# Kernel optimization log

Measured on AMD Instinct MI355X. Metric: run time of the kernel, lower is better.

Reference implementation:

```python
import jax, jax.numpy as jnp
import numpy as np

VOCAB, EMBED, UNITS, BATCH, SEQ = 32000, 1024, 1024, 64, 128


def _lstm_layer(x, mask, Wx, Wh, b):
    """Keras-style LSTM (gate order i, f, g, o) with zero-masking semantics.
    x: [B, T, D], mask: [B, T] bool. Returns (seq [B,T,U], h [B,U], c [B,U])."""
    B, T, _ = x.shape
    U = Wh.shape[0]
    # Precompute input projection for all timesteps (big GEMM, compute-bound).
    xp = jnp.einsum('btd,dg->btg', x, Wx) + b            # [B, T, 4U]
    xp_t = jnp.transpose(xp, (1, 0, 2))                  # [T, B, 4U]
    mask_t = jnp.transpose(mask, (1, 0))                 # [T, B]

    def step(carry, inp):
        h, c = carry
        xt, mt = inp
        z = xt + h @ Wh                                  # [B, 4U]
        i = jax.nn.sigmoid(z[:, :U])
        f = jax.nn.sigmoid(z[:, U:2 * U])
        g = jnp.tanh(z[:, 2 * U:3 * U])
        o = jax.nn.sigmoid(z[:, 3 * U:])
        c_new = f * c + i * g
        h_new = o * jnp.tanh(c_new)
        m = mt[:, None]
        h2 = jnp.where(m, h_new, h)   # masked steps carry state/output through
        c2 = jnp.where(m, c_new, c)
        return (h2, c2), h2

    h0 = jnp.zeros((B, U), x.dtype)
    c0 = jnp.zeros((B, U), x.dtype)
    (h, c), seq_t = jax.lax.scan(step, (h0, c0), (xp_t, mask_t))
    return jnp.transpose(seq_t, (1, 0, 2)), h, c


def setup_inputs() -> dict:
    key = jax.random.key(0)
    ks = jax.random.split(key, 8)
    inputs = jax.random.randint(ks[0], (BATCH, SEQ), 0, VOCAB, dtype=jnp.int32)
    emb = jax.random.uniform(ks[1], (VOCAB, EMBED), jnp.float32, -0.05, 0.05)
    s_in = 1.0 / np.sqrt(EMBED)
    s_u = 1.0 / np.sqrt(UNITS)
    Wx0 = jax.random.normal(ks[2], (EMBED, 4 * UNITS), jnp.float32) * s_in
    Wh0 = jax.random.normal(ks[3], (UNITS, 4 * UNITS), jnp.float32) * s_u
    b0 = jnp.zeros((4 * UNITS,), jnp.float32).at[UNITS:2 * UNITS].set(1.0)  # unit_forget_bias
    Wx1 = jax.random.normal(ks[4], (UNITS, 4 * UNITS), jnp.float32) * s_u
    Wh1 = jax.random.normal(ks[5], (UNITS, 4 * UNITS), jnp.float32) * s_u
    b1 = jnp.zeros((4 * UNITS,), jnp.float32).at[UNITS:2 * UNITS].set(1.0)
    return {"inputs": inputs, "emb": emb, "Wx0": Wx0, "Wh0": Wh0, "b0": b0,
            "Wx1": Wx1, "Wh1": Wh1, "b1": b1}


def reference(inputs, emb, Wx0, Wh0, b0, Wx1, Wh1, b1):
    mask = inputs != 0                              # mask_zero=True
    x = emb[inputs]                                 # [B, T, E]
    seq, h0_, c0_ = _lstm_layer(x, mask, Wx0, Wh0, b0)
    seq, h1_, c1_ = _lstm_layer(seq, mask, Wx1, Wh1, b1)
    return seq, h0_, c0_, h1_, c1_
```

## Files before the change

### kernel.cpp

```cpp
#include <hip/hip_runtime.h>
#include <hip/hip_bf16.h>
#include <cstdint>
#include <cstddef>

typedef __attribute__((ext_vector_type(8))) short bf16x8;
typedef __attribute__((ext_vector_type(4))) float f32x4;
typedef __attribute__((ext_vector_type(4))) unsigned int u32x4;

__device__ __forceinline__ unsigned short f2bf(float f) {
  unsigned u = __float_as_uint(f);
  return (unsigned short)((u + 0x7fffu + ((u >> 16) & 1u)) >> 16);
}

__global__ __launch_bounds__(256) void transpose_cast_k(const float* __restrict__ W,
                                                        unsigned short* __restrict__ WT) {
  __shared__ float tile[32][33];
  const int bn = blockIdx.x * 32, bk = blockIdx.y * 32;
  const int tx = threadIdx.x & 31, ty = threadIdx.x >> 5;
#pragma unroll
  for (int i = 0; i < 4; ++i) {
    const int k = ty + i * 8;
    tile[k][tx] = W[(size_t)(bk + k) * 4096 + bn + tx];
  }
  __syncthreads();
#pragma unroll
  for (int i = 0; i < 4; ++i) {
    const int n = ty + i * 8;
    WT[(size_t)(bn + n) * 1024 + bk + tx] = f2bf(tile[tx][n]);
  }
}

__global__ __launch_bounds__(256) void embed_gather_k(const int* __restrict__ ids,
                                                      const float* __restrict__ emb,
                                                      unsigned short* __restrict__ x) {
  const int bt = blockIdx.x;
  const int id = ids[bt];
  const float4 v = ((const float4*)(emb + (size_t)id * 1024))[threadIdx.x];
  union { unsigned short u[4]; unsigned long long ll; } o;
  o.u[0] = f2bf(v.x); o.u[1] = f2bf(v.y); o.u[2] = f2bf(v.z); o.u[3] = f2bf(v.w);
  *(unsigned long long*)(x + (size_t)bt * 1024 + threadIdx.x * 4) = o.ll;
}

__global__ __launch_bounds__(256) void gemm_bt_k(const unsigned short* __restrict__ A,
                                                 const unsigned short* __restrict__ BT,
                                                 const float* __restrict__ bias,
                                                 float* __restrict__ C) {
  __shared__ char sA[128 * 128];
  __shared__ char sB[128 * 128];
  const int bid = blockIdx.x;
  const int bm = (bid >> 5) * 128;
  const int bn = (bid & 31) * 128;
  const int tid = threadIdx.x, lane = tid & 63;
  const int wv = tid >> 6, wm = wv >> 1, wn = wv & 1;
  const int lrow = lane & 15, lk = (lane >> 4) * 16;
  f32x4 acc[4][4] = {};
  for (int kt = 0; kt < 16; ++kt) {
    const int k0 = kt * 64;
    bf16x8 av[4], bv[4];
#pragma unroll
    for (int i = 0; i < 4; ++i) {
      const int ch = i * 256 + tid;
      const int row = ch >> 3, c = ch & 7;
      av[i] = *(const bf16x8*)(A + (size_t)(bm + row) * 1024 + k0 + c * 8);
      bv[i] = *(const bf16x8*)(BT + (size_t)(bn + row) * 1024 + k0 + c * 8);
    }
    __syncthreads();
#pragma unroll
    for (int i = 0; i < 4; ++i) {
      const int ch = i * 256 + tid;
      const int row = ch >> 3, c = ch & 7;
      const int off = row * 128 + ((c * 16) ^ ((row & 7) << 4));
      *(bf16x8*)(sA + off) = av[i];
      *(bf16x8*)(sB + off) = bv[i];
    }
    __syncthreads();
#pragma unroll
    for (int kk = 0; kk < 2; ++kk) {
      bf16x8 af[4], bf_[4];
#pragma unroll
      for (int mi = 0; mi < 4; ++mi) {
        const int row = wm * 64 + mi * 16 + lrow;
        af[mi] = *(const bf16x8*)(sA + row * 128 + ((kk * 64 + lk) ^ ((row & 7) << 4)));
      }
#pragma unroll
      for (int ni = 0; ni < 4; ++ni) {
        const int row = wn * 64 + ni * 16 + lrow;
        bf_[ni] = *(const bf16x8*)(sB + row * 128 + ((kk * 64 + lk) ^ ((row & 7) << 4)));
      }
#pragma unroll
      for (int mi = 0; mi < 4; ++mi)
#pragma unroll
        for (int ni = 0; ni < 4; ++ni)
          acc[mi][ni] = __builtin_amdgcn_mfma_f32_16x16x32_bf16(af[mi], bf_[ni], acc[mi][ni], 0, 0, 0);
    }
  }
  const int cr0 = (lane >> 4) * 4;
#pragma unroll
  for (int mi = 0; mi < 4; ++mi)
#pragma unroll
    for (int ni = 0; ni < 4; ++ni) {
      const int col = bn + wn * 64 + ni * 16 + lrow;
      const float bb = bias[col];
#pragma unroll
      for (int r = 0; r < 4; ++r) {
        const int row = bm + wm * 64 + mi * 16 + cr0 + r;
        C[(size_t)row * 4096 + col] = acc[mi][ni][r] + bb;
      }
    }
}

template <int LAYER>
__global__ __launch_bounds__(256) void lstm_layer_k(
    const float* __restrict__ xp,
    const unsigned short* __restrict__ WhT,
    const int* __restrict__ ids,
    unsigned short* __restrict__ hbuf,
    unsigned short* __restrict__ seqbf,
    float* __restrict__ seqf,
    float* __restrict__ hfin, float* __restrict__ cfin,
    unsigned* __restrict__ flags_all) {
  extern __shared__ __align__(16) char dlds[];
  char* wlds = dlds;
  float* zp = (float*)(dlds + 131072);
  const int tid = threadIdx.x, lane = tid & 63, wave = tid >> 6;
  const int wg = blockIdx.x;
  const int g = wg & 3, w = wg >> 2;
  const int b0 = g * 16, u0 = w * 16;
  unsigned* flags = flags_all + g * 1024;

  for (int i = 0; i < 32; ++i) {
    const int ch = i * 256 + tid;
    const int n = ch >> 7, c = ch & 127;
    const int grow = (n >> 4) * 1024 + u0 + (n & 15);
    bf16x8 v = *(const bf16x8*)(WhT + (size_t)grow * 1024 + c * 8);
    *(bf16x8*)(wlds + n * 2048 + ((c * 16) ^ ((n & 7) << 4))) = v;
  }
  const int rrow = tid >> 4, du = tid & 15;
  const int brow = b0 + rrow, unit = u0 + du;
  {
    unsigned short* p = hbuf + (size_t)brow * 1024 + unit;
    unsigned zv = 0;
    asm volatile("global_store_short %0, %1, off sc0 sc1" :: "v"(p), "v"(zv) : "memory");
  }
  asm volatile("s_waitcnt vmcnt(0)" ::: "memory");
  __syncthreads();
  if (tid == 0)
    __hip_atomic_store(&flags[w * 16], 1u, __ATOMIC_RELAXED, __HIP_MEMORY_SCOPE_AGENT);

  float c_reg = 0.f, h_reg = 0.f;
  const int lr = lane & 15;
  const int lkb = (lane >> 4) * 16;
  const int wq = wave * 512;

  for (int t = 0; t < 128; ++t) {
    const float* xr = xp + ((size_t)brow * 128 + t) * 4096 + unit;
    const float x0 = xr[0], x1 = xr[1024], x2 = xr[2048], x3 = xr[3072];
    const int idv = ids[brow * 128 + t];
    {
      const unsigned* fp = flags + lane * 16;
      const unsigned target = (unsigned)(t + 1);
      for (;;) {
        unsigned v = __hip_atomic_load(fp, __ATOMIC_RELAXED, __HIP_MEMORY_SCOPE_AGENT);
        if (__all((int)(v >= target))) break;
        __builtin_amdgcn_s_sleep(1);
      }
    }
    const char* hb = (const char*)hbuf + (size_t)(t & 1) * 131072 +
                     (size_t)(b0 + lr) * 2048 + wq + lkb;
    u32x4 araw[8];
#pragma unroll
    for (int c = 0; c < 8; ++c)
      asm volatile("global_load_dwordx4 %0, %1, off sc0 sc1"
                   : "=&v"(araw[c]) : "v"(hb + c * 64) : "memory");
    asm volatile("s_waitcnt vmcnt(0)" ::: "memory");
    __builtin_amdgcn_sched_barrier(0);
    f32x4 acc[4] = {};
#pragma unroll
    for (int gg = 0; gg < 4; ++gg) {
      const int n = gg * 16 + lr;
      const char* bb = wlds + n * 2048;
      const int bx = (n & 7) << 4;
#pragma unroll
      for (int c = 0; c < 8; ++c) {
        bf16x8 bfv = *(const bf16x8*)(bb + ((wq + c * 64 + lkb) ^ bx));
        acc[gg] = __builtin_amdgcn_mfma_f32_16x16x32_bf16(
            __builtin_bit_cast(bf16x8, araw[c]), bfv, acc[gg], 0, 0, 0);
      }
    }
    const int zr0 = (lane >> 4) * 4;
#pragma unroll
    for (int gg = 0; gg < 4; ++gg)
#pragma unroll
      for (int r = 0; r < 4; ++r)
        zp[((wave * 4 + gg) * 16 + zr0 + r) * 20 + lr] = acc[gg][r];
    __syncthreads();
    float zg0 = x0, zg1 = x1, zg2 = x2, zg3 = x3;
#pragma unroll
    for (int ww = 0; ww < 4; ++ww) {
      zg0 += zp[((ww * 4 + 0) * 16 + rrow) * 20 + du];
      zg1 += zp[((ww * 4 + 1) * 16 + rrow) * 20 + du];
      zg2 += zp[((ww * 4 + 2) * 16 + rrow) * 20 + du];
      zg3 += zp[((ww * 4 + 3) * 16 + rrow) * 20 + du];
    }
    const float ig = 1.f / (1.f + __expf(-zg0));
    const float fg = 1.f / (1.f + __expf(-zg1));
    const float gt = 1.f - 2.f / (1.f + __expf(2.f * zg2));
    const float og = 1.f / (1.f + __expf(-zg3));
    const float cn = fg * c_reg + ig * gt;
    const float hn = og * (1.f - 2.f / (1.f + __expf(2.f * cn)));
    if (idv != 0) { c_reg = cn; h_reg = hn; }
    const unsigned short hb16 = f2bf(h_reg);
    {
      unsigned short* p = hbuf + (size_t)((t & 1) ^ 1) * 65536 + (size_t)brow * 1024 + unit;
      asm volatile("global_store_short %0, %1, off sc0 sc1"
                   :: "v"(p), "v"((unsigned)hb16) : "memory");
    }
    if (LAYER == 0)
      seqbf[((size_t)brow * 128 + t) * 1024 + unit] = hb16;
    else
      seqf[((size_t)brow * 128 + t) * 1024 + unit] = h_reg;
    asm volatile("s_waitcnt vmcnt(0)" ::: "memory");
    __syncthreads();
    if (tid == 0)
      __hip_atomic_store(&flags[w * 16], (unsigned)(t + 2), __ATOMIC_RELAXED,
                         __HIP_MEMORY_SCOPE_AGENT);
  }
  hfin[(size_t)brow * 1024 + unit] = h_reg;
  cfin[(size_t)brow * 1024 + unit] = c_reg;
}

extern "C" void kernel_launch(void* const* d_in, const int* in_sizes, int n_in,
                              void* d_out, int out_size, void* d_ws, size_t ws_size,
                              hipStream_t stream) {
  (void)in_sizes; (void)n_in; (void)out_size; (void)ws_size;
  const int* ids = (const int*)d_in[0];
  const float* emb = (const float*)d_in[1];
  const float* Wx0 = (const float*)d_in[2];
  const float* Wh0 = (const float*)d_in[3];
  const float* b0 = (const float*)d_in[4];
  const float* Wx1 = (const float*)d_in[5];
  const float* Wh1 = (const float*)d_in[6];
  const float* b1 = (const float*)d_in[7];
  float* out = (float*)d_out;

  char* ws = (char*)d_ws;
  const size_t SZ_WT = (size_t)4096 * 1024 * 2;
  unsigned short* WxT0 = (unsigned short*)(ws);
  unsigned short* WhT0 = (unsigned short*)(ws + SZ_WT);
  unsigned short* WxT1 = (unsigned short*)(ws + 2 * SZ_WT);
  unsigned short* WhT1 = (unsigned short*)(ws + 3 * SZ_WT);
  unsigned short* xbf = (unsigned short*)(ws + 4 * SZ_WT);
  unsigned short* seq0 = (unsigned short*)(ws + 4 * SZ_WT + 16777216);
  unsigned short* hbuf = (unsigned short*)(ws + 4 * SZ_WT + 2 * 16777216);
  unsigned* flags = (unsigned*)(ws + 4 * SZ_WT + 2 * 16777216 + 262144);
  float* xpb = (float*)(ws + 4 * SZ_WT + 2 * 16777216 + 262144 + 16384);

  float* h0f = out + 8388608;
  float* c0f = h0f + 65536;
  float* h1f = c0f + 65536;
  float* c1f = h1f + 65536;

  transpose_cast_k<<<dim3(128, 32), dim3(256), 0, stream>>>(Wx0, WxT0);
  transpose_cast_k<<<dim3(128, 32), dim3(256), 0, stream>>>(Wh0, WhT0);
  transpose_cast_k<<<dim3(128, 32), dim3(256), 0, stream>>>(Wx1, WxT1);
  transpose_cast_k<<<dim3(128, 32), dim3(256), 0, stream>>>(Wh1, WhT1);
  embed_gather_k<<<dim3(8192), dim3(256), 0, stream>>>(ids, emb, xbf);
  gemm_bt_k<<<dim3(2048), dim3(256), 0, stream>>>(xbf, WxT0, b0, xpb);

  hipFuncSetAttribute(reinterpret_cast<const void*>(&lstm_layer_k<0>),
                      hipFuncAttributeMaxDynamicSharedMemorySize, 151552);
  hipFuncSetAttribute(reinterpret_cast<const void*>(&lstm_layer_k<1>),
                      hipFuncAttributeMaxDynamicSharedMemorySize, 151552);

  hipMemsetAsync(flags, 0, 16384, stream);
  {
    const float* xp_p = xpb;
    const unsigned short* wht = WhT0;
    const int* ids_p = ids;
    unsigned short* hb_p = hbuf;
    unsigned short* sb_p = seq0;
    float* sf_p = nullptr;
    float* hf_p = h0f;
    float* cf_p = c0f;
    unsigned* fl_p = flags;
    void* ka[9] = {&xp_p, &wht, &ids_p, &hb_p, &sb_p, &sf_p, &hf_p, &cf_p, &fl_p};
    hipLaunchCooperativeKernel(reinterpret_cast<const void*>(&lstm_layer_k<0>),
                               dim3(256), dim3(256), ka, 151552u, stream);
  }
  gemm_bt_k<<<dim3(2048), dim3(256), 0, stream>>>(seq0, WxT1, b1, xpb);
  hipMemsetAsync(flags, 0, 16384, stream);
  {
    const float* xp_p = xpb;
    const unsigned short* wht = WhT1;
    const int* ids_p = ids;
    unsigned short* hb_p = hbuf;
    unsigned short* sb_p = nullptr;
    float* sf_p = out;
    float* hf_p = h1f;
    float* cf_p = c1f;
    unsigned* fl_p = flags;
    void* ka[9] = {&xp_p, &wht, &ids_p, &hb_p, &sb_p, &sf_p, &hf_p, &cf_p, &fl_p};
    hipLaunchCooperativeKernel(reinterpret_cast<const void*>(&lstm_layer_k<1>),
                               dim3(256), dim3(256), ka, 151552u, stream);
  }
}
```

Measured before the change: 1.388 ms.

## Replace flag-based step sync with self-validating h packets carrying step tags

The per-step cross-workgroup handshake moves off separate flag words. Each h value is now published as a 16-byte packet holding four bf16 hidden units plus a step tag. Consumers poll the packets directly and reload only those whose tag is stale, then stage the h tile through LDS for the MFMA. This drops the separate flag store/poll round trip, the vmcnt wait before each flag publish and the flag memsets. In exchange it doubles the size of the h exchange buffer, adds extra LDS staging and block barriers, and leaves the gate math on a single wave that handles four units per lane.

```diff
diff --git a/kernel.cpp b/kernel.cpp
--- a/kernel.cpp
+++ b/kernel.cpp
@@ -6,6 +6,7 @@
 typedef __attribute__((ext_vector_type(8))) short bf16x8;
 typedef __attribute__((ext_vector_type(4))) float f32x4;
 typedef __attribute__((ext_vector_type(4))) unsigned int u32x4;
+typedef __attribute__((ext_vector_type(2))) unsigned int u32x2;
 
 __device__ __forceinline__ unsigned short f2bf(float f) {
   unsigned u = __float_as_uint(f);
@@ -114,19 +115,19 @@
     const float* __restrict__ xp,
     const unsigned short* __restrict__ WhT,
     const int* __restrict__ ids,
-    unsigned short* __restrict__ hbuf,
+    u32x4* __restrict__ pktbuf,
     unsigned short* __restrict__ seqbf,
     float* __restrict__ seqf,
-    float* __restrict__ hfin, float* __restrict__ cfin,
-    unsigned* __restrict__ flags_all) {
+    float* __restrict__ hfin, float* __restrict__ cfin) {
   extern __shared__ __align__(16) char dlds[];
   char* wlds = dlds;
-  float* zp = (float*)(dlds + 131072);
+  char* htile = dlds + 131072;
+  float* zp = (float*)htile;
   const int tid = threadIdx.x, lane = tid & 63, wave = tid >> 6;
   const int wg = blockIdx.x;
   const int g = wg & 3, w = wg >> 2;
   const int b0 = g * 16, u0 = w * 16;
-  unsigned* flags = flags_all + g * 1024;
+  constexpr unsigned EB = LAYER * 512u;
 
   for (int i = 0; i < 32; ++i) {
     const int ch = i * 256 + tid;
@@ -135,45 +136,69 @@
     bf16x8 v = *(const bf16x8*)(WhT + (size_t)grow * 1024 + c * 8);
     *(bf16x8*)(wlds + n * 2048 + ((c * 16) ^ ((n & 7) << 4))) = v;
   }
-  const int rrow = tid >> 4, du = tid & 15;
-  const int brow = b0 + rrow, unit = u0 + du;
-  {
-    unsigned short* p = hbuf + (size_t)brow * 1024 + unit;
-    unsigned zv = 0;
-    asm volatile("global_store_short %0, %1, off sc0 sc1" :: "v"(p), "v"(zv) : "memory");
-  }
-  asm volatile("s_waitcnt vmcnt(0)" ::: "memory");
+
+  const int prow = lane >> 2, pk4 = lane & 3;
+  const int brow = b0 + prow;
+  const int myunit = u0 + pk4 * 4;
+  float cc[4] = {0.f, 0.f, 0.f, 0.f}, hh[4] = {0.f, 0.f, 0.f, 0.f};
+
+  if (wave == 0) {
+    u32x4 z; z[0] = 0u; z[1] = 0u; z[2] = EB + 1u; z[3] = 0u;
+    u32x4* p = pktbuf + (size_t)brow * 256 + (u0 >> 2) + pk4;
+    asm volatile("global_store_dwordx4 %0, %1, off sc0 sc1" :: "v"(p), "v"(z) : "memory");
+  }
   __syncthreads();
-  if (tid == 0)
-    __hip_atomic_store(&flags[w * 16], 1u, __ATOMIC_RELAXED, __HIP_MEMORY_SCOPE_AGENT);
-
-  float c_reg = 0.f, h_reg = 0.f;
-  const int lr = lane & 15;
-  const int lkb = (lane >> 4) * 16;
-  const int wq = wave * 512;
+
+  const int crow = tid >> 4;
+  const int cpk0 = tid & 15;
+  const int lr = lane & 15, lkb = (lane >> 4) * 16, wq = wave * 512;
+  const int asw = (lr & 7) << 4;
 
   for (int t = 0; t < 128; ++t) {
-    const float* xr = xp + ((size_t)brow * 128 + t) * 4096 + unit;
-    const float x0 = xr[0], x1 = xr[1024], x2 = xr[2048], x3 = xr[3072];
-    const int idv = ids[brow * 128 + t];
-    {
-      const unsigned* fp = flags + lane * 16;
-      const unsigned target = (unsigned)(t + 1);
-      for (;;) {
-        unsigned v = __hip_atomic_load(fp, __ATOMIC_RELAXED, __HIP_MEMORY_SCOPE_AGENT);
-        if (__all((int)(v >= target))) break;
-        __builtin_amdgcn_s_sleep(1);
-      }
-    }
-    const char* hb = (const char*)hbuf + (size_t)(t & 1) * 131072 +
-                     (size_t)(b0 + lr) * 2048 + wq + lkb;
-    u32x4 araw[8];
+    __syncthreads();
+    f32x4 xq0 = {}, xq1 = {}, xq2 = {}, xq3 = {};
+    int idv = 0;
+    if (wave == 0) {
+      const float* xr = xp + ((size_t)brow * 128 + t) * 4096 + myunit;
+      xq0 = *(const f32x4*)(xr);
+      xq1 = *(const f32x4*)(xr + 1024);
+      xq2 = *(const f32x4*)(xr + 2048);
+      xq3 = *(const f32x4*)(xr + 3072);
+      idv = ids[brow * 128 + t];
+    }
+    const unsigned target = EB + (unsigned)t + 1u;
+    const char* pb = (const char*)pktbuf + (size_t)(t & 1) * 262144 +
+                     ((size_t)(b0 + crow) * 256 + cpk0) * 16;
+    u32x4 pkt[16];
+#pragma unroll
+    for (int i = 0; i < 16; ++i)
+      asm volatile("global_load_dwordx4 %0, %1, off sc0 sc1"
+                   : "=&v"(pkt[i]) : "v"(pb + i * 256) : "memory");
+    asm volatile("s_waitcnt vmcnt(0)" ::: "memory");
+    for (;;) {
+      bool again = false;
+#pragma unroll
+      for (int i = 0; i < 16; ++i)
+        if (pkt[i][2] != target) {
+          asm volatile("global_load_dwordx4 %0, %1, off sc0 sc1"
+                       : "=&v"(pkt[i]) : "v"(pb + i * 256) : "memory");
+          again = true;
+        }
+      if (!again) break;
+      asm volatile("s_waitcnt vmcnt(0)" ::: "memory");
+    }
+    __builtin_amdgcn_sched_barrier(0);
+#pragma unroll
+    for (int i = 0; i < 16; ++i) {
+      const int pk = cpk0 + 16 * i;
+      u32x2 v; v[0] = pkt[i][0]; v[1] = pkt[i][1];
+      *(u32x2*)(htile + crow * 2048 + ((pk * 8) ^ ((crow & 7) << 4))) = v;
+    }
+    __syncthreads();
+    bf16x8 af[8];
 #pragma unroll
     for (int c = 0; c < 8; ++c)
-      asm volatile("global_load_dwordx4 %0, %1, off sc0 sc1"
-                   : "=&v"(araw[c]) : "v"(hb + c * 64) : "memory");
-    asm volatile("s_waitcnt vmcnt(0)" ::: "memory");
-    __builtin_amdgcn_sched_barrier(0);
+      af[c] = *(const bf16x8*)(htile + lr * 2048 + ((wq + c * 64 + lkb) ^ asw));
     f32x4 acc[4] = {};
 #pragma unroll
     for (int gg = 0; gg < 4; ++gg) {
@@ -183,10 +208,10 @@
 #pragma unroll
       for (int c = 0; c < 8; ++c) {
         bf16x8 bfv = *(const bf16x8*)(bb + ((wq + c * 64 + lkb) ^ bx));
-        acc[gg] = __builtin_amdgcn_mfma_f32_16x16x32_bf16(
-            __builtin_bit_cast(bf16x8, araw[c]), bfv, acc[gg], 0, 0, 0);
-      }
-    }
+        acc[gg] = __builtin_amdgcn_mfma_f32_16x16x32_bf16(af[c], bfv, acc[gg], 0, 0, 0);
+      }
+    }
+    __syncthreads();
     const int zr0 = (lane >> 4) * 4;
 #pragma unroll
     for (int gg = 0; gg < 4; ++gg)
@@ -194,39 +219,47 @@
       for (int r = 0; r < 4; ++r)
         zp[((wave * 4 + gg) * 16 + zr0 + r) * 20 + lr] = acc[gg][r];
     __syncthreads();
-    float zg0 = x0, zg1 = x1, zg2 = x2, zg3 = x3;
-#pragma unroll
-    for (int ww = 0; ww < 4; ++ww) {
-      zg0 += zp[((ww * 4 + 0) * 16 + rrow) * 20 + du];
-      zg1 += zp[((ww * 4 + 1) * 16 + rrow) * 20 + du];
-      zg2 += zp[((ww * 4 + 2) * 16 + rrow) * 20 + du];
-      zg3 += zp[((ww * 4 + 3) * 16 + rrow) * 20 + du];
-    }
-    const float ig = 1.f / (1.f + __expf(-zg0));
-    const float fg = 1.f / (1.f + __expf(-zg1));
-    const float gt = 1.f - 2.f / (1.f + __expf(2.f * zg2));
-    const float og = 1.f / (1.f + __expf(-zg3));
-    const float cn = fg * c_reg + ig * gt;
-    const float hn = og * (1.f - 2.f / (1.f + __expf(2.f * cn)));
-    if (idv != 0) { c_reg = cn; h_reg = hn; }
-    const unsigned short hb16 = f2bf(h_reg);
-    {
-      unsigned short* p = hbuf + (size_t)((t & 1) ^ 1) * 65536 + (size_t)brow * 1024 + unit;
-      asm volatile("global_store_short %0, %1, off sc0 sc1"
-                   :: "v"(p), "v"((unsigned)hb16) : "memory");
-    }
-    if (LAYER == 0)
-      seqbf[((size_t)brow * 128 + t) * 1024 + unit] = hb16;
-    else
-      seqf[((size_t)brow * 128 + t) * 1024 + unit] = h_reg;
-    asm volatile("s_waitcnt vmcnt(0)" ::: "memory");
-    __syncthreads();
-    if (tid == 0)
-      __hip_atomic_store(&flags[w * 16], (unsigned)(t + 2), __ATOMIC_RELAXED,
-                         __HIP_MEMORY_SCOPE_AGENT);
-  }
-  hfin[(size_t)brow * 1024 + unit] = h_reg;
-  cfin[(size_t)brow * 1024 + unit] = c_reg;
+    if (wave == 0) {
+      f32x4 zs0 = xq0, zs1 = xq1, zs2 = xq2, zs3 = xq3;
+#pragma unroll
+      for (int ww = 0; ww < 4; ++ww) {
+        zs0 += *(const f32x4*)(zp + ((ww * 4 + 0) * 16 + prow) * 20 + pk4 * 4);
+        zs1 += *(const f32x4*)(zp + ((ww * 4 + 1) * 16 + prow) * 20 + pk4 * 4);
+        zs2 += *(const f32x4*)(zp + ((ww * 4 + 2) * 16 + prow) * 20 + pk4 * 4);
+        zs3 += *(const f32x4*)(zp + ((ww * 4 + 3) * 16 + prow) * 20 + pk4 * 4);
+      }
+#pragma unroll
+      for (int u = 0; u < 4; ++u) {
+        const float ig = 1.f / (1.f + __expf(-zs0[u]));
+        const float fg = 1.f / (1.f + __expf(-zs1[u]));
+        const float gt = 1.f - 2.f / (1.f + __expf(2.f * zs2[u]));
+        const float og = 1.f / (1.f + __expf(-zs3[u]));
+        const float cn = fg * cc[u] + ig * gt;
+        const float hn = og * (1.f - 2.f / (1.f + __expf(2.f * cn)));
+        if (idv != 0) { cc[u] = cn; hh[u] = hn; }
+      }
+      const unsigned p01 = (unsigned)f2bf(hh[0]) | ((unsigned)f2bf(hh[1]) << 16);
+      const unsigned p23 = (unsigned)f2bf(hh[2]) | ((unsigned)f2bf(hh[3]) << 16);
+      u32x4 op; op[0] = p01; op[1] = p23; op[2] = EB + (unsigned)t + 2u; op[3] = 0u;
+      u32x4* dst = pktbuf + (size_t)((t + 1) & 1) * 16384 + (size_t)brow * 256 +
+                   (u0 >> 2) + pk4;
+      asm volatile("global_store_dwordx4 %0, %1, off sc0 sc1" :: "v"(dst), "v"(op) : "memory");
+      if (LAYER == 0) {
+        u32x2 sv; sv[0] = p01; sv[1] = p23;
+        *(u32x2*)(seqbf + ((size_t)brow * 128 + t) * 1024 + myunit) = sv;
+      } else {
+        f32x4 sv; sv[0] = hh[0]; sv[1] = hh[1]; sv[2] = hh[2]; sv[3] = hh[3];
+        *(f32x4*)(seqf + ((size_t)brow * 128 + t) * 1024 + myunit) = sv;
+      }
+    }
+  }
+  if (wave == 0) {
+    f32x4 hv, cv;
+#pragma unroll
+    for (int u = 0; u < 4; ++u) { hv[u] = hh[u]; cv[u] = cc[u]; }
+    *(f32x4*)(hfin + (size_t)brow * 1024 + myunit) = hv;
+    *(f32x4*)(cfin + (size_t)brow * 1024 + myunit) = cv;
+  }
 }
 
 extern "C" void kernel_launch(void* const* d_in, const int* in_sizes, int n_in,
@@ -251,9 +284,8 @@
   unsigned short* WhT1 = (unsigned short*)(ws + 3 * SZ_WT);
   unsigned short* xbf = (unsigned short*)(ws + 4 * SZ_WT);
   unsigned short* seq0 = (unsigned short*)(ws + 4 * SZ_WT + 16777216);
-  unsigned short* hbuf = (unsigned short*)(ws + 4 * SZ_WT + 2 * 16777216);
-  unsigned* flags = (unsigned*)(ws + 4 * SZ_WT + 2 * 16777216 + 262144);
-  float* xpb = (float*)(ws + 4 * SZ_WT + 2 * 16777216 + 262144 + 16384);
+  u32x4* pktbuf = (u32x4*)(ws + 4 * SZ_WT + 2 * 16777216);
+  float* xpb = (float*)(ws + 4 * SZ_WT + 2 * 16777216 + 524288);
 
   float* h0f = out + 8388608;
   float* c0f = h0f + 65536;
@@ -268,39 +300,35 @@
   gemm_bt_k<<<dim3(2048), dim3(256), 0, stream>>>(xbf, WxT0, b0, xpb);
 
   hipFuncSetAttribute(reinterpret_cast<const void*>(&lstm_layer_k<0>),
-                      hipFuncAttributeMaxDynamicSharedMemorySize, 151552);
+                      hipFuncAttributeMaxDynamicSharedMemorySize, 163840);
   hipFuncSetAttribute(reinterpret_cast<const void*>(&lstm_layer_k<1>),
-                      hipFuncAttributeMaxDynamicSharedMemorySize, 151552);
-
-  hipMemsetAsync(flags, 0, 16384, stream);
+                      hipFuncAttributeMaxDynamicSharedMemorySize, 163840);
+
   {
     const float* xp_p = xpb;
     const unsigned short* wht = WhT0;
     const int* ids_p = ids;
-    unsigned short* hb_p = hbuf;
+    u32x4* pb_p = pktbuf;
     unsigned short* sb_p = seq0;
     float* sf_p = nullptr;
     float* hf_p = h0f;
     float* cf_p = c0f;
-    unsigned* fl_p = flags;
-    void* ka[9] = {&xp_p, &wht, &ids_p, &hb_p, &sb_p, &sf_p, &hf_p, &cf_p, &fl_p};
+    void* ka[8] = {&xp_p, &wht, &ids_p, &pb_p, &sb_p, &sf_p, &hf_p, &cf_p};
     hipLaunchCooperativeKernel(reinterpret_cast<const void*>(&lstm_layer_k<0>),
-                               dim3(256), dim3(256), ka, 151552u, stream);
+                               dim3(256), dim3(256), ka, 163840u, stream);
   }
   gemm_bt_k<<<dim3(2048), dim3(256), 0, stream>>>(seq0, WxT1, b1, xpb);
-  hipMemsetAsync(flags, 0, 16384, stream);
   {
     const float* xp_p = xpb;
     const unsigned short* wht = WhT1;
     const int* ids_p = ids;
-    unsigned short* hb_p = hbuf;
+    u32x4* pb_p = pktbuf;
     unsigned short* sb_p = nullptr;
     float* sf_p = out;
     float* hf_p = h1f;
     float* cf_p = c1f;
-    unsigned* fl_p = flags;
-    void* ka[9] = {&xp_p, &wht, &ids_p, &hb_p, &sb_p, &sf_p, &hf_p, &cf_p, &fl_p};
+    void* ka[8] = {&xp_p, &wht, &ids_p, &pb_p, &sb_p, &sf_p, &hf_p, &cf_p};
     hipLaunchCooperativeKernel(reinterpret_cast<const void*>(&lstm_layer_k<1>),
-                               dim3(256), dim3(256), ka, 151552u, stream);
-  }
-}
+                               dim3(256), dim3(256), ka, 163840u, stream);
+  }
+}
```

After: 1.415 ms. No clear change (+2.0%).
